# Optimization experiments

Measured on AMD Instinct MI355X. Metric: run time of the kernel, lower is better.

The kernel has to match this reference:

```python
import jax, jax.numpy as jnp
import numpy as np

B, T, E, H, V, D, C = 16384, 128, 32, 128, 30001, 128, 3


def setup_inputs() -> dict:
    key = jax.random.key(0)
    ks = jax.random.split(key, 8)
    tokens = jax.random.randint(ks[0], (B, T), 0, V, dtype=jnp.int32)
    emb = jax.random.normal(ks[1], (V, E), jnp.float32) * 0.05
    W = jax.random.normal(ks[2], (E, 3 * H), jnp.float32) * (1.0 / np.sqrt(E))
    U = jax.random.normal(ks[3], (H, 3 * H), jnp.float32) * (1.0 / np.sqrt(H))
    b = jnp.zeros((2, 3 * H), jnp.float32)  # [input_bias, recurrent_bias] (reset_after=True)
    W1 = jax.random.normal(ks[4], (H, D), jnp.float32) * (1.0 / np.sqrt(H))
    b1 = jnp.zeros((D,), jnp.float32)
    Wout = jax.random.normal(ks[5], (D, C), jnp.float32) * (1.0 / np.sqrt(D))
    bout = jnp.zeros((C,), jnp.float32)
    return {"tokens": tokens, "emb": emb, "W": W, "U": U, "b": b,
            "W1": W1, "b1": b1, "Wout": Wout, "bout": bout}


def _gru_masked(x, mask, W, U, b):
    # x: [B,T,E], mask: [B,T] bool. Keras GRU defaults: reset_after=True,
    # activation=tanh, recurrent_activation=sigmoid. Masked steps freeze state.
    xp = jnp.einsum('bte,eg->btg', x, W) + b[0]  # precompute input projections [B,T,3H]

    def step(h, inp):
        xg, m = inp                      # xg: [B,3H], m: [B]
        rec = h @ U + b[1]               # [B,3H]
        z = jax.nn.sigmoid(xg[:, :H] + rec[:, :H])
        r = jax.nn.sigmoid(xg[:, H:2 * H] + rec[:, H:2 * H])
        hh = jnp.tanh(xg[:, 2 * H:] + r * rec[:, 2 * H:])
        h_new = z * h + (1.0 - z) * hh
        h = jnp.where(m[:, None], h_new, h)
        return h, None

    h0 = jnp.zeros((x.shape[0], H), x.dtype)
    h, _ = jax.lax.scan(step, h0, (jnp.swapaxes(xp, 0, 1), jnp.swapaxes(mask, 0, 1)))
    return h


def reference(tokens, emb, W, U, b, W1, b1, Wout, bout):
    x = emb[tokens]                      # [B,T,E] embedding lookup
    mask = tokens != 0                   # mask_zero=True
    h = _gru_masked(x, mask, W, U, b)    # [B,H]
    d = h @ W1 + b1
    d = d * jax.nn.sigmoid(d)            # swish
    logits = d @ Wout + bout
    return jax.nn.softmax(logits, axis=-1)
```

## Files before the change

kernel.cpp:

```cpp
#include <hip/hip_runtime.h>
#include <hip/hip_fp16.h>

#define B_ 16384
#define T_ 128
#define E_ 32
#define H_ 128
#define G3_ 384
#define V_ 30001
#define D_ 128
#define C_ 3

#define LOG2E 1.44269504088896340736f

typedef _Float16 f16;
typedef f16 f16x4 __attribute__((ext_vector_type(4)));
typedef f16 f16x8 __attribute__((ext_vector_type(8)));
typedef float f32x4 __attribute__((ext_vector_type(4)));
typedef unsigned int u32;

#define HPITCH   272
#define H0_OFF   0
#define H1_OFF   4352
#define TOK_OFF  8704
#define DBUF_OFF 16896
#define LDS_TOTAL 25344

__device__ __forceinline__ float frcp_(float x)  { return __builtin_amdgcn_rcpf(x); }
__device__ __forceinline__ float fexp2_(float x) { return __builtin_amdgcn_exp2f(x); }

#define BAR_LGKM() asm volatile("s_waitcnt lgkmcnt(0)\n\ts_barrier" ::: "memory")

#define K1_ROWS 8
__global__ __launch_bounds__(384) void embw_kernel(
    const float* __restrict__ emb,
    const float* __restrict__ W,
    const float* __restrict__ b,
    f16* __restrict__ embW)
{
    __shared__ float sW[E_][G3_];
    __shared__ float sE[K1_ROWS][E_];
    const int g = threadIdx.x;
    #pragma unroll
    for (int e = 0; e < E_; ++e) sW[e][g] = W[e * G3_ + g];
    const int v0 = blockIdx.x * K1_ROWS;
    for (int idx = g; idx < K1_ROWS * E_; idx += 384) {
        int rr = idx >> 5, ee = idx & 31;
        int v = v0 + rr;
        sE[rr][ee] = (v < V_) ? emb[v * E_ + ee] : 0.f;
    }
    __syncthreads();
    const float bg = b[g] + ((g < 256) ? b[G3_ + g] : 0.f);
    const float sc = (g >= 256) ? (2.f * LOG2E) : (-LOG2E);
    #pragma unroll
    for (int rr = 0; rr < K1_ROWS; ++rr) {
        int v = v0 + rr;
        if (v >= V_) break;
        float acc = bg;
        #pragma unroll
        for (int e = 0; e < E_; ++e) acc = fmaf(sE[rr][e], sW[e][g], acc);
        embW[(size_t)v * G3_ + g] = (f16)(acc * sc);
    }
}

__global__ __launch_bounds__(512, 4) void gru_mfma_kernel(
    const int*   __restrict__ tokens,
    const f16*   __restrict__ embW,
    const float* __restrict__ U,
    const float* __restrict__ b,
    const float* __restrict__ W1,
    const float* __restrict__ b1,
    const float* __restrict__ Wout,
    const float* __restrict__ bout,
    float* __restrict__ out)
{
    __shared__ char lds[LDS_TOTAL];
    const int tid = threadIdx.x;
    const int w   = tid >> 6;
    const int l   = tid & 63;
    const int cl  = l & 15;
    const int q   = l >> 4;
    const int R0  = blockIdx.x * 16;
    const int c0  = w * 16 + 4 * q;

    for (int idx = tid; idx < 16 * T_; idx += 512) {
        int r = idx >> 7, t = idx & 127;
        u32 tok = (u32)tokens[(size_t)(R0 + r) * T_ + t];
        *(u32*)(&lds[TOK_OFF + t * 64 + r * 4]) = tok * 768u;
    }
    for (int idx = tid; idx < H1_OFF / 4; idx += 512)
        ((float*)(lds + H0_OFF))[idx] = 0.f;

    f16x8 Af[3][4];
    #pragma unroll
    for (int gt = 0; gt < 3; ++gt) {
        const float sc = (gt == 2) ? (2.f * LOG2E) : (-LOG2E);
        const int n = gt * 128 + w * 16 + cl;
        #pragma unroll
        for (int kt = 0; kt < 4; ++kt) {
            const int k0 = kt * 32 + q * 8;
            f16x8 fr;
            #pragma unroll
            for (int j = 0; j < 8; ++j)
                fr[j] = (f16)(U[(size_t)(k0 + j) * G3_ + n] * sc);
            Af[gt][kt] = fr;
        }
    }

    f32x4 bh4;
    #pragma unroll
    for (int i = 0; i < 4; ++i)
        bh4[i] = 2.f * LOG2E * b[G3_ + 256 + c0 + i];

    float hreg[4];
    #pragma unroll
    for (int i = 0; i < 4; ++i) hreg[i] = 0.f;

    __syncthreads();

    const char* embWb = (const char*)embW;
    const int colb = c0 * 2;

    u32 offc = *(const u32*)(&lds[TOK_OFF + cl * 4]);
    f16x4 xzc = *(const f16x4*)(embWb + offc + colb);
    f16x4 xrc = *(const f16x4*)(embWb + offc + colb + 256);
    f16x4 xhc = *(const f16x4*)(embWb + offc + colb + 512);

    int cur = 0;
    for (int t = 0; t < T_; ++t) {
        const char* hb = lds + (cur ? H1_OFF : H0_OFF);
        char*       hn = lds + (cur ? H0_OFF : H1_OFF);

        u32 offn = offc;
        f16x4 xzn = xzc, xrn = xrc, xhn = xhc;
        if (t + 1 < T_) {
            offn = *(const u32*)(&lds[TOK_OFF + (t + 1) * 64 + cl * 4]);
            xzn = *(const f16x4*)(embWb + offn + colb);
            xrn = *(const f16x4*)(embWb + offn + colb + 256);
            xhn = *(const f16x4*)(embWb + offn + colb + 512);
        }

        const f16x8 bf0 = *(const f16x8*)(hb + cl * HPITCH + q * 16);
        const f16x8 bf1 = *(const f16x8*)(hb + cl * HPITCH + q * 16 + 64);
        const f16x8 bf2 = *(const f16x8*)(hb + cl * HPITCH + q * 16 + 128);
        const f16x8 bf3 = *(const f16x8*)(hb + cl * HPITCH + q * 16 + 192);

        f32x4 xz4, xr4;
        #pragma unroll
        for (int i = 0; i < 4; ++i) { xz4[i] = (float)xzc[i]; xr4[i] = (float)xrc[i]; }
        f32x4 accz = __builtin_amdgcn_mfma_f32_16x16x32_f16(Af[0][0], bf0, xz4, 0, 0, 0);
        f32x4 accr = __builtin_amdgcn_mfma_f32_16x16x32_f16(Af[1][0], bf0, xr4, 0, 0, 0);
        f32x4 acch = __builtin_amdgcn_mfma_f32_16x16x32_f16(Af[2][0], bf0, bh4, 0, 0, 0);
        accz = __builtin_amdgcn_mfma_f32_16x16x32_f16(Af[0][1], bf1, accz, 0, 0, 0);
        accr = __builtin_amdgcn_mfma_f32_16x16x32_f16(Af[1][1], bf1, accr, 0, 0, 0);
        acch = __builtin_amdgcn_mfma_f32_16x16x32_f16(Af[2][1], bf1, acch, 0, 0, 0);
        accz = __builtin_amdgcn_mfma_f32_16x16x32_f16(Af[0][2], bf2, accz, 0, 0, 0);
        accr = __builtin_amdgcn_mfma_f32_16x16x32_f16(Af[1][2], bf2, accr, 0, 0, 0);
        acch = __builtin_amdgcn_mfma_f32_16x16x32_f16(Af[2][2], bf2, acch, 0, 0, 0);
        accz = __builtin_amdgcn_mfma_f32_16x16x32_f16(Af[0][3], bf3, accz, 0, 0, 0);
        accr = __builtin_amdgcn_mfma_f32_16x16x32_f16(Af[1][3], bf3, accr, 0, 0, 0);
        acch = __builtin_amdgcn_mfma_f32_16x16x32_f16(Af[2][3], bf3, acch, 0, 0, 0);

        f16x4 hv4;
        #pragma unroll
        for (int i = 0; i < 4; ++i) {
            const float z  = frcp_(1.f + fexp2_(accz[i]));
            const float r  = frcp_(1.f + fexp2_(accr[i]));
            const float hh = fmaf(-2.f, frcp_(1.f + fexp2_(fmaf(r, acch[i], (float)xhc[i]))), 1.f);
            const float hv = hreg[i];
            float nv = fmaf(z, hv - hh, hh);
            nv = (offc != 0u) ? nv : hv;
            hreg[i] = nv;
            hv4[i] = (f16)nv;
        }
        *(f16x4*)(hn + cl * HPITCH + colb) = hv4;

        BAR_LGKM();
        cur ^= 1;
        offc = offn; xzc = xzn; xrc = xrn; xhc = xhn;
    }

    {
        f16x8 Wf[4];
        #pragma unroll
        for (int kt = 0; kt < 4; ++kt) {
            const int k0 = kt * 32 + q * 8;
            f16x8 fr;
            #pragma unroll
            for (int j = 0; j < 8; ++j)
                fr[j] = (f16)W1[(size_t)(k0 + j) * D_ + w * 16 + cl];
            Wf[kt] = fr;
        }
        const char* hb = lds + H0_OFF;
        f32x4 bd4;
        #pragma unroll
        for (int i = 0; i < 4; ++i) bd4[i] = b1[c0 + i];
        const f16x8 bf0 = *(const f16x8*)(hb + cl * HPITCH + q * 16);
        const f16x8 bf1 = *(const f16x8*)(hb + cl * HPITCH + q * 16 + 64);
        const f16x8 bf2 = *(const f16x8*)(hb + cl * HPITCH + q * 16 + 128);
        const f16x8 bf3 = *(const f16x8*)(hb + cl * HPITCH + q * 16 + 192);
        f32x4 dacc = __builtin_amdgcn_mfma_f32_16x16x32_f16(Wf[0], bf0, bd4, 0, 0, 0);
        dacc = __builtin_amdgcn_mfma_f32_16x16x32_f16(Wf[1], bf1, dacc, 0, 0, 0);
        dacc = __builtin_amdgcn_mfma_f32_16x16x32_f16(Wf[2], bf2, dacc, 0, 0, 0);
        dacc = __builtin_amdgcn_mfma_f32_16x16x32_f16(Wf[3], bf3, dacc, 0, 0, 0);
        f32x4 sw4;
        #pragma unroll
        for (int i = 0; i < 4; ++i) {
            const float v = dacc[i];
            sw4[i] = v * frcp_(1.f + fexp2_(-LOG2E * v));
        }
        *(f32x4*)(&lds[DBUF_OFF + cl * 528 + c0 * 4]) = sw4;
    }
    __syncthreads();

    if (w == 0 && l < 48) {
        const int row = l & 15, ci = l >> 4;
        float acc = bout[ci];
        #pragma unroll 4
        for (int k = 0; k < D_; ++k)
            acc = fmaf(*(const float*)(&lds[DBUF_OFF + row * 528 + k * 4]),
                       Wout[k * 3 + ci], acc);
        const float v0 = __shfl(acc, row);
        const float v1 = __shfl(acc, row + 16);
        const float v2 = __shfl(acc, row + 32);
        const float mx = fmaxf(v0, fmaxf(v1, v2));
        const float e0 = fexp2_(LOG2E * (v0 - mx));
        const float e1 = fexp2_(LOG2E * (v1 - mx));
        const float e2 = fexp2_(LOG2E * (v2 - mx));
        const float inv = frcp_(e0 + e1 + e2);
        const float mine = (ci == 0) ? e0 : (ci == 1) ? e1 : e2;
        out[(size_t)(R0 + row) * 3 + ci] = mine * inv;
    }
}

extern "C" void kernel_launch(void* const* d_in, const int* in_sizes, int n_in,
                              void* d_out, int out_size, void* d_ws, size_t ws_size,
                              hipStream_t stream) {
    (void)in_sizes; (void)n_in; (void)out_size; (void)ws_size;
    const int*   tokens = (const int*)d_in[0];
    const float* emb    = (const float*)d_in[1];
    const float* W      = (const float*)d_in[2];
    const float* U      = (const float*)d_in[3];
    const float* b      = (const float*)d_in[4];
    const float* W1     = (const float*)d_in[5];
    const float* b1     = (const float*)d_in[6];
    const float* Wout   = (const float*)d_in[7];
    const float* bout   = (const float*)d_in[8];
    float* out  = (float*)d_out;
    f16*   embW = (f16*)d_ws;

    hipLaunchKernelGGL(embw_kernel, dim3((V_ + K1_ROWS - 1) / K1_ROWS), dim3(384), 0, stream,
                       emb, W, b, embW);
    hipLaunchKernelGGL(gru_mfma_kernel, dim3(B_ / 16), dim3(512), 0, stream,
                       tokens, embW, U, b, W1, b1, Wout, bout, out);
}
```

Baseline: 395.4 us.

## Process two independent 16-row groups per block to interleave GRU recurrences

```diff
diff --git a/kernel.cpp b/kernel.cpp
--- a/kernel.cpp
+++ b/kernel.cpp
@@ -22,8 +22,9 @@
 #define H0_OFF   0
 #define H1_OFF   4352
 #define TOK_OFF  8704
-#define DBUF_OFF 16896
-#define LDS_TOTAL 25344
+#define GRP_BYTES 16960
+#define DBUF_OFF  33920
+#define LDS_TOTAL 50816
 
 __device__ __forceinline__ float frcp_(float x)  { return __builtin_amdgcn_rcpf(x); }
 __device__ __forceinline__ float fexp2_(float x) { return __builtin_amdgcn_exp2f(x); }
@@ -62,7 +63,7 @@
     }
 }
 
-__global__ __launch_bounds__(512, 4) void gru_mfma_kernel(
+__global__ __launch_bounds__(512, 3) void gru_mfma_kernel(
     const int*   __restrict__ tokens,
     const f16*   __restrict__ embW,
     const float* __restrict__ U,
@@ -79,16 +80,23 @@
     const int l   = tid & 63;
     const int cl  = l & 15;
     const int q   = l >> 4;
-    const int R0  = blockIdx.x * 16;
+    const int R0  = blockIdx.x * 32;
     const int c0  = w * 16 + 4 * q;
 
-    for (int idx = tid; idx < 16 * T_; idx += 512) {
+    char* gA = lds;
+    char* gB = lds + GRP_BYTES;
+
+    for (int idx = tid; idx < 32 * T_; idx += 512) {
         int r = idx >> 7, t = idx & 127;
         u32 tok = (u32)tokens[(size_t)(R0 + r) * T_ + t];
-        *(u32*)(&lds[TOK_OFF + t * 64 + r * 4]) = tok * 768u;
-    }
-    for (int idx = tid; idx < H1_OFF / 4; idx += 512)
-        ((float*)(lds + H0_OFF))[idx] = 0.f;
+        *(u32*)(&lds[(r >> 4) * GRP_BYTES + TOK_OFF + t * 64 + (r & 15) * 4]) = tok * 768u;
+    }
+    if (tid < 32)
+        *(u32*)(&lds[(tid >> 4) * GRP_BYTES + TOK_OFF + 128 * 64 + (tid & 15) * 4]) = 0u;
+    for (int idx = tid; idx < 1088; idx += 512) {
+        ((float*)(gA + H0_OFF))[idx] = 0.f;
+        ((float*)(gB + H0_OFF))[idx] = 0.f;
+    }
 
     f16x8 Af[3][4];
     #pragma unroll
@@ -111,72 +119,108 @@
     for (int i = 0; i < 4; ++i)
         bh4[i] = 2.f * LOG2E * b[G3_ + 256 + c0 + i];
 
-    float hreg[4];
-    #pragma unroll
-    for (int i = 0; i < 4; ++i) hreg[i] = 0.f;
+    float hregA[4], hregB[4];
+    #pragma unroll
+    for (int i = 0; i < 4; ++i) { hregA[i] = 0.f; hregB[i] = 0.f; }
 
     __syncthreads();
 
     const char* embWb = (const char*)embW;
     const int colb = c0 * 2;
 
-    u32 offc = *(const u32*)(&lds[TOK_OFF + cl * 4]);
-    f16x4 xzc = *(const f16x4*)(embWb + offc + colb);
-    f16x4 xrc = *(const f16x4*)(embWb + offc + colb + 256);
-    f16x4 xhc = *(const f16x4*)(embWb + offc + colb + 512);
+    u32 offA = *(const u32*)(gA + TOK_OFF + cl * 4);
+    u32 offB = *(const u32*)(gB + TOK_OFF + cl * 4);
+    f16x4 xzA = *(const f16x4*)(embWb + offA + colb);
+    f16x4 xrA = *(const f16x4*)(embWb + offA + colb + 256);
+    f16x4 xhA = *(const f16x4*)(embWb + offA + colb + 512);
+    f16x4 xzB = *(const f16x4*)(embWb + offB + colb);
+    f16x4 xrB = *(const f16x4*)(embWb + offB + colb + 256);
+    f16x4 xhB = *(const f16x4*)(embWb + offB + colb + 512);
 
     int cur = 0;
     for (int t = 0; t < T_; ++t) {
-        const char* hb = lds + (cur ? H1_OFF : H0_OFF);
-        char*       hn = lds + (cur ? H0_OFF : H1_OFF);
-
-        u32 offn = offc;
-        f16x4 xzn = xzc, xrn = xrc, xhn = xhc;
-        if (t + 1 < T_) {
-            offn = *(const u32*)(&lds[TOK_OFF + (t + 1) * 64 + cl * 4]);
-            xzn = *(const f16x4*)(embWb + offn + colb);
-            xrn = *(const f16x4*)(embWb + offn + colb + 256);
-            xhn = *(const f16x4*)(embWb + offn + colb + 512);
-        }
-
-        const f16x8 bf0 = *(const f16x8*)(hb + cl * HPITCH + q * 16);
-        const f16x8 bf1 = *(const f16x8*)(hb + cl * HPITCH + q * 16 + 64);
-        const f16x8 bf2 = *(const f16x8*)(hb + cl * HPITCH + q * 16 + 128);
-        const f16x8 bf3 = *(const f16x8*)(hb + cl * HPITCH + q * 16 + 192);
-
-        f32x4 xz4, xr4;
-        #pragma unroll
-        for (int i = 0; i < 4; ++i) { xz4[i] = (float)xzc[i]; xr4[i] = (float)xrc[i]; }
-        f32x4 accz = __builtin_amdgcn_mfma_f32_16x16x32_f16(Af[0][0], bf0, xz4, 0, 0, 0);
-        f32x4 accr = __builtin_amdgcn_mfma_f32_16x16x32_f16(Af[1][0], bf0, xr4, 0, 0, 0);
-        f32x4 acch = __builtin_amdgcn_mfma_f32_16x16x32_f16(Af[2][0], bf0, bh4, 0, 0, 0);
-        accz = __builtin_amdgcn_mfma_f32_16x16x32_f16(Af[0][1], bf1, accz, 0, 0, 0);
-        accr = __builtin_amdgcn_mfma_f32_16x16x32_f16(Af[1][1], bf1, accr, 0, 0, 0);
-        acch = __builtin_amdgcn_mfma_f32_16x16x32_f16(Af[2][1], bf1, acch, 0, 0, 0);
-        accz = __builtin_amdgcn_mfma_f32_16x16x32_f16(Af[0][2], bf2, accz, 0, 0, 0);
-        accr = __builtin_amdgcn_mfma_f32_16x16x32_f16(Af[1][2], bf2, accr, 0, 0, 0);
-        acch = __builtin_amdgcn_mfma_f32_16x16x32_f16(Af[2][2], bf2, acch, 0, 0, 0);
-        accz = __builtin_amdgcn_mfma_f32_16x16x32_f16(Af[0][3], bf3, accz, 0, 0, 0);
-        accr = __builtin_amdgcn_mfma_f32_16x16x32_f16(Af[1][3], bf3, accr, 0, 0, 0);
-        acch = __builtin_amdgcn_mfma_f32_16x16x32_f16(Af[2][3], bf3, acch, 0, 0, 0);
-
-        f16x4 hv4;
+        const char* hbA = gA + (cur ? H1_OFF : H0_OFF);
+        char*       hnA = gA + (cur ? H0_OFF : H1_OFF);
+        const char* hbB = gB + (cur ? H1_OFF : H0_OFF);
+        char*       hnB = gB + (cur ? H0_OFF : H1_OFF);
+
+        const u32 offAn = *(const u32*)(gA + TOK_OFF + (t + 1) * 64 + cl * 4);
+        const u32 offBn = *(const u32*)(gB + TOK_OFF + (t + 1) * 64 + cl * 4);
+        const f16x4 xzAn = *(const f16x4*)(embWb + offAn + colb);
+        const f16x4 xrAn = *(const f16x4*)(embWb + offAn + colb + 256);
+        const f16x4 xhAn = *(const f16x4*)(embWb + offAn + colb + 512);
+        const f16x4 xzBn = *(const f16x4*)(embWb + offBn + colb);
+        const f16x4 xrBn = *(const f16x4*)(embWb + offBn + colb + 256);
+        const f16x4 xhBn = *(const f16x4*)(embWb + offBn + colb + 512);
+
+        const f16x8 aA0 = *(const f16x8*)(hbA + cl * HPITCH + q * 16);
+        const f16x8 aA1 = *(const f16x8*)(hbA + cl * HPITCH + q * 16 + 64);
+        const f16x8 aA2 = *(const f16x8*)(hbA + cl * HPITCH + q * 16 + 128);
+        const f16x8 aA3 = *(const f16x8*)(hbA + cl * HPITCH + q * 16 + 192);
+        const f16x8 aB0 = *(const f16x8*)(hbB + cl * HPITCH + q * 16);
+        const f16x8 aB1 = *(const f16x8*)(hbB + cl * HPITCH + q * 16 + 64);
+        const f16x8 aB2 = *(const f16x8*)(hbB + cl * HPITCH + q * 16 + 128);
+        const f16x8 aB3 = *(const f16x8*)(hbB + cl * HPITCH + q * 16 + 192);
+
+        f32x4 xz4A, xr4A, xz4B, xr4B;
         #pragma unroll
         for (int i = 0; i < 4; ++i) {
-            const float z  = frcp_(1.f + fexp2_(accz[i]));
-            const float r  = frcp_(1.f + fexp2_(accr[i]));
-            const float hh = fmaf(-2.f, frcp_(1.f + fexp2_(fmaf(r, acch[i], (float)xhc[i]))), 1.f);
-            const float hv = hreg[i];
-            float nv = fmaf(z, hv - hh, hh);
-            nv = (offc != 0u) ? nv : hv;
-            hreg[i] = nv;
-            hv4[i] = (f16)nv;
-        }
-        *(f16x4*)(hn + cl * HPITCH + colb) = hv4;
+            xz4A[i] = (float)xzA[i]; xr4A[i] = (float)xrA[i];
+            xz4B[i] = (float)xzB[i]; xr4B[i] = (float)xrB[i];
+        }
+        f32x4 azA = __builtin_amdgcn_mfma_f32_16x16x32_f16(Af[0][0], aA0, xz4A, 0, 0, 0);
+        f32x4 arA = __builtin_amdgcn_mfma_f32_16x16x32_f16(Af[1][0], aA0, xr4A, 0, 0, 0);
+        f32x4 ahA = __builtin_amdgcn_mfma_f32_16x16x32_f16(Af[2][0], aA0, bh4,  0, 0, 0);
+        f32x4 azB = __builtin_amdgcn_mfma_f32_16x16x32_f16(Af[0][0], aB0, xz4B, 0, 0, 0);
+        f32x4 arB = __builtin_amdgcn_mfma_f32_16x16x32_f16(Af[1][0], aB0, xr4B, 0, 0, 0);
+        f32x4 ahB = __builtin_amdgcn_mfma_f32_16x16x32_f16(Af[2][0], aB0, bh4,  0, 0, 0);
+        azA = __builtin_amdgcn_mfma_f32_16x16x32_f16(Af[0][1], aA1, azA, 0, 0, 0);
+        arA = __builtin_amdgcn_mfma_f32_16x16x32_f16(Af[1][1], aA1, arA, 0, 0, 0);
+        ahA = __builtin_amdgcn_mfma_f32_16x16x32_f16(Af[2][1], aA1, ahA, 0, 0, 0);
+        azB = __builtin_amdgcn_mfma_f32_16x16x32_f16(Af[0][1], aB1, azB, 0, 0, 0);
+        arB = __builtin_amdgcn_mfma_f32_16x16x32_f16(Af[1][1], aB1, arB, 0, 0, 0);
+        ahB = __builtin_amdgcn_mfma_f32_16x16x32_f16(Af[2][1], aB1, ahB, 0, 0, 0);
+        azA = __builtin_amdgcn_mfma_f32_16x16x32_f16(Af[0][2], aA2, azA, 0, 0, 0);
+        arA = __builtin_amdgcn_mfma_f32_16x16x32_f16(Af[1][2], aA2, arA, 0, 0, 0);
+        ahA = __builtin_amdgcn_mfma_f32_16x16x32_f16(Af[2][2], aA2, ahA, 0, 0, 0);
+        azB = __builtin_amdgcn_mfma_f32_16x16x32_f16(Af[0][2], aB2, azB, 0, 0, 0);
+        arB = __builtin_amdgcn_mfma_f32_16x16x32_f16(Af[1][2], aB2, arB, 0, 0, 0);
+        ahB = __builtin_amdgcn_mfma_f32_16x16x32_f16(Af[2][2], aB2, ahB, 0, 0, 0);
+        azA = __builtin_amdgcn_mfma_f32_16x16x32_f16(Af[0][3], aA3, azA, 0, 0, 0);
+        arA = __builtin_amdgcn_mfma_f32_16x16x32_f16(Af[1][3], aA3, arA, 0, 0, 0);
+        ahA = __builtin_amdgcn_mfma_f32_16x16x32_f16(Af[2][3], aA3, ahA, 0, 0, 0);
+        azB = __builtin_amdgcn_mfma_f32_16x16x32_f16(Af[0][3], aB3, azB, 0, 0, 0);
+        arB = __builtin_amdgcn_mfma_f32_16x16x32_f16(Af[1][3], aB3, arB, 0, 0, 0);
+        ahB = __builtin_amdgcn_mfma_f32_16x16x32_f16(Af[2][3], aB3, ahB, 0, 0, 0);
+
+        f16x4 hv4A, hv4B;
+        #pragma unroll
+        for (int i = 0; i < 4; ++i) {
+            const float zA  = frcp_(1.f + fexp2_(azA[i]));
+            const float rA  = frcp_(1.f + fexp2_(arA[i]));
+            const float hhA = fmaf(-2.f, frcp_(1.f + fexp2_(fmaf(rA, ahA[i], (float)xhA[i]))), 1.f);
+            const float hvA = hregA[i];
+            float nvA = fmaf(zA, hvA - hhA, hhA);
+            nvA = (offA != 0u) ? nvA : hvA;
+            hregA[i] = nvA;
+            hv4A[i] = (f16)nvA;
+
+            const float zB  = frcp_(1.f + fexp2_(azB[i]));
+            const float rB  = frcp_(1.f + fexp2_(arB[i]));
+            const float hhB = fmaf(-2.f, frcp_(1.f + fexp2_(fmaf(rB, ahB[i], (float)xhB[i]))), 1.f);
+            const float hvB = hregB[i];
+            float nvB = fmaf(zB, hvB - hhB, hhB);
+            nvB = (offB != 0u) ? nvB : hvB;
+            hregB[i] = nvB;
+            hv4B[i] = (f16)nvB;
+        }
+        *(f16x4*)(hnA + cl * HPITCH + colb) = hv4A;
+        *(f16x4*)(hnB + cl * HPITCH + colb) = hv4B;
 
         BAR_LGKM();
         cur ^= 1;
-        offc = offn; xzc = xzn; xrc = xrn; xhc = xhn;
+        offA = offAn; xzA = xzAn; xrA = xrAn; xhA = xhAn;
+        offB = offBn; xzB = xzBn; xrB = xrBn; xhB = xhBn;
     }
 
     {
@@ -190,38 +234,54 @@
                 fr[j] = (f16)W1[(size_t)(k0 + j) * D_ + w * 16 + cl];
             Wf[kt] = fr;
         }
-        const char* hb = lds + H0_OFF;
         f32x4 bd4;
         #pragma unroll
         for (int i = 0; i < 4; ++i) bd4[i] = b1[c0 + i];
-        const f16x8 bf0 = *(const f16x8*)(hb + cl * HPITCH + q * 16);
-        const f16x8 bf1 = *(const f16x8*)(hb + cl * HPITCH + q * 16 + 64);
-        const f16x8 bf2 = *(const f16x8*)(hb + cl * HPITCH + q * 16 + 128);
-        const f16x8 bf3 = *(const f16x8*)(hb + cl * HPITCH + q * 16 + 192);
-        f32x4 dacc = __builtin_amdgcn_mfma_f32_16x16x32_f16(Wf[0], bf0, bd4, 0, 0, 0);
-        dacc = __builtin_amdgcn_mfma_f32_16x16x32_f16(Wf[1], bf1, dacc, 0, 0, 0);
-        dacc = __builtin_amdgcn_mfma_f32_16x16x32_f16(Wf[2], bf2, dacc, 0, 0, 0);
-        dacc = __builtin_amdgcn_mfma_f32_16x16x32_f16(Wf[3], bf3, dacc, 0, 0, 0);
-        f32x4 sw4;
+
+        const char* hbA = gA + H0_OFF;
+        const char* hbB = gB + H0_OFF;
+        const f16x8 aA0 = *(const f16x8*)(hbA + cl * HPITCH + q * 16);
+        const f16x8 aA1 = *(const f16x8*)(hbA + cl * HPITCH + q * 16 + 64);
+        const f16x8 aA2 = *(const f16x8*)(hbA + cl * HPITCH + q * 16 + 128);
+        const f16x8 aA3 = *(const f16x8*)(hbA + cl * HPITCH + q * 16 + 192);
+        const f16x8 aB0 = *(const f16x8*)(hbB + cl * HPITCH + q * 16);
+        const f16x8 aB1 = *(const f16x8*)(hbB + cl * HPITCH + q * 16 + 64);
+        const f16x8 aB2 = *(const f16x8*)(hbB + cl * HPITCH + q * 16 + 128);
+        const f16x8 aB3 = *(const f16x8*)(hbB + cl * HPITCH + q * 16 + 192);
+        f32x4 dA = __builtin_amdgcn_mfma_f32_16x16x32_f16(Wf[0], aA0, bd4, 0, 0, 0);
+        f32x4 dB = __builtin_amdgcn_mfma_f32_16x16x32_f16(Wf[0], aB0, bd4, 0, 0, 0);
+        dA = __builtin_amdgcn_mfma_f32_16x16x32_f16(Wf[1], aA1, dA, 0, 0, 0);
+        dB = __builtin_amdgcn_mfma_f32_16x16x32_f16(Wf[1], aB1, dB, 0, 0, 0);
+        dA = __builtin_amdgcn_mfma_f32_16x16x32_f16(Wf[2], aA2, dA, 0, 0, 0);
+        dB = __builtin_amdgcn_mfma_f32_16x16x32_f16(Wf[2], aB2, dB, 0, 0, 0);
+        dA = __builtin_amdgcn_mfma_f32_16x16x32_f16(Wf[3], aA3, dA, 0, 0, 0);
+        dB = __builtin_amdgcn_mfma_f32_16x16x32_f16(Wf[3], aB3, dB, 0, 0, 0);
+
+        f32x4 swA, swB;
         #pragma unroll
         for (int i = 0; i < 4; ++i) {
-            const float v = dacc[i];
-            sw4[i] = v * frcp_(1.f + fexp2_(-LOG2E * v));
-        }
-        *(f32x4*)(&lds[DBUF_OFF + cl * 528 + c0 * 4]) = sw4;
+            const float vA = dA[i];
+            const float vB = dB[i];
+            swA[i] = vA * frcp_(1.f + fexp2_(-LOG2E * vA));
+            swB[i] = vB * frcp_(1.f + fexp2_(-LOG2E * vB));
+        }
+        *(f32x4*)(&lds[DBUF_OFF + cl * 528 + c0 * 4]) = swA;
+        *(f32x4*)(&lds[DBUF_OFF + (16 + cl) * 528 + c0 * 4]) = swB;
     }
     __syncthreads();
 
-    if (w == 0 && l < 48) {
-        const int row = l & 15, ci = l >> 4;
+    if (w < 2 && l < 48) {
+        const int row = (l & 15) + 16 * w;
+        const int ci  = l >> 4;
         float acc = bout[ci];
         #pragma unroll 4
         for (int k = 0; k < D_; ++k)
             acc = fmaf(*(const float*)(&lds[DBUF_OFF + row * 528 + k * 4]),
                        Wout[k * 3 + ci], acc);
-        const float v0 = __shfl(acc, row);
-        const float v1 = __shfl(acc, row + 16);
-        const float v2 = __shfl(acc, row + 32);
+        const int rl = l & 15;
+        const float v0 = __shfl(acc, rl);
+        const float v1 = __shfl(acc, rl + 16);
+        const float v2 = __shfl(acc, rl + 32);
         const float mx = fmaxf(v0, fmaxf(v1, v2));
         const float e0 = fexp2_(LOG2E * (v0 - mx));
         const float e1 = fexp2_(LOG2E * (v1 - mx));
@@ -250,6 +310,6 @@
 
     hipLaunchKernelGGL(embw_kernel, dim3((V_ + K1_ROWS - 1) / K1_ROWS), dim3(384), 0, stream,
                        emb, W, b, embW);
-    hipLaunchKernelGGL(gru_mfma_kernel, dim3(B_ / 16), dim3(512), 0, stream,
+    hipLaunchKernelGGL(gru_mfma_kernel, dim3(B_ / 32), dim3(512), 0, stream,
                        tokens, embW, U, b, W1, b1, Wout, bout, out);
 }
```

Measured after the change: 388.8 us. Within noise of the previous version (-1.7%).
